# Performance work log

Hardware: AMD Instinct MI355X
Metric: run time of the kernel (lower is better)

The kernel has to match this reference:

```python
import jax, jax.numpy as jnp
import numpy as np

EPS_BN = 1e-5
EPS_LN = 1e-5


def _conv1d(x, w, b, pad):
    # x: (B, Cin, L), w: (Cout, Cin, K)
    y = jax.lax.conv_general_dilated(x, w, window_strides=(1,), padding=[(pad, pad)],
                                     dimension_numbers=('NCH', 'OIH', 'NCH'))
    return y + b[None, :, None]


def _bn_eval(x, g, b, m, v):
    return (x - m[None, :, None]) * (g / jnp.sqrt(v + EPS_BN))[None, :, None] + b[None, :, None]


def _maxpool2(x):
    B, C, L = x.shape
    return x.reshape(B, C, L // 2, 2).max(-1)


def _wavelet(x, t, s, w):
    # x: (B, In); t, s, w: (Out, In); mexican_hat wavelet
    z = (x[:, None, :] - t[None]) / (s + 1e-8)  # (B, Out, In)
    wav = (1.0 - z * z) * jnp.exp(-0.5 * z * z)
    return jnp.einsum('boi,oi->bo', wav, w)


def _ln(x, g, b):
    m = x.mean(-1, keepdims=True)
    v = ((x - m) ** 2).mean(-1, keepdims=True)
    return (x - m) / jnp.sqrt(v + EPS_LN) * g + b


def setup_inputs() -> dict:
    key = jax.random.key(0)
    ks = iter(jax.random.split(key, 40))
    B, L = 1024, 1024
    R = 64                 # repr_dim
    KIN = 128 * (R // 4)   # 2048 = conv stem flattened features
    d = {}
    d['x'] = jax.random.normal(next(ks), (B, 1, L), jnp.float32)
    for i, (ci, co, k) in enumerate([(1, 32, 7), (32, 64, 5), (64, 128, 3)], 1):
        fan = ci * k
        d[f'conv{i}_w'] = jax.random.normal(next(ks), (co, ci, k), jnp.float32) / np.sqrt(fan)
        d[f'conv{i}_b'] = jnp.zeros((co,), jnp.float32)
        d[f'bn{i}_g'] = jnp.ones((co,), jnp.float32)
        d[f'bn{i}_b'] = jnp.zeros((co,), jnp.float32)
        d[f'bn{i}_m'] = jax.random.normal(next(ks), (co,), jnp.float32) * 0.1
        d[f'bn{i}_v'] = jax.random.uniform(next(ks), (co,), jnp.float32, 0.5, 1.5)
    for i, fin in enumerate([KIN, R, R], 1):
        d[f'wl{i}_t'] = jax.random.uniform(next(ks), (R, fin), jnp.float32, -1.0, 1.0)
        d[f'wl{i}_s'] = jax.random.uniform(next(ks), (R, fin), jnp.float32, 0.1, 1.0)
        d[f'wl{i}_w'] = jax.random.normal(next(ks), (R, fin), jnp.float32) / np.sqrt(fin)
        d[f'ln{i}_g'] = jnp.ones((R,), jnp.float32)
        d[f'ln{i}_b'] = jnp.zeros((R,), jnp.float32)
    return d


def _forward(x, p):
    h = _conv1d(x, p['conv1_w'], p['conv1_b'], 3)
    h = jax.nn.gelu(_bn_eval(h, p['bn1_g'], p['bn1_b'], p['bn1_m'], p['bn1_v']), approximate=False)
    h = _maxpool2(h)
    h = _conv1d(h, p['conv2_w'], p['conv2_b'], 2)
    h = jax.nn.gelu(_bn_eval(h, p['bn2_g'], p['bn2_b'], p['bn2_m'], p['bn2_v']), approximate=False)
    h = _maxpool2(h)
    h = _conv1d(h, p['conv3_w'], p['conv3_b'], 1)
    h = jax.nn.gelu(_bn_eval(h, p['bn3_g'], p['bn3_b'], p['bn3_m'], p['bn3_v']), approximate=False)
    # AdaptiveAvgPool1d(16): L=256 splits evenly into 16 bins of 16
    B, C, L = h.shape
    h = h.reshape(B, C, 16, L // 16).mean(-1)
    feat = h.reshape(B, -1)  # (B, 2048)
    for i in (1, 2, 3):
        feat = _ln(jax.nn.silu(_wavelet(feat, p[f'wl{i}_t'], p[f'wl{i}_s'], p[f'wl{i}_w'])),
                   p[f'ln{i}_g'], p[f'ln{i}_b'])
    return feat  # (B, 64)


def reference(x, conv1_w, conv1_b, bn1_g, bn1_b, bn1_m, bn1_v,
              conv2_w, conv2_b, bn2_g, bn2_b, bn2_m, bn2_v,
              conv3_w, conv3_b, bn3_g, bn3_b, bn3_m, bn3_v,
              wl1_t, wl1_s, wl1_w, ln1_g, ln1_b,
              wl2_t, wl2_s, wl2_w, ln2_g, ln2_b,
              wl3_t, wl3_s, wl3_w, ln3_g, ln3_b):
    p = dict(locals())
    p.pop('x')
    return _forward(x, p)
```

## Files before the change

### kernel.cpp

```cpp
#include <hip/hip_runtime.h>
#include <hip/hip_bf16.h>
#include <math.h>

#define WS_W2H   0
#define WS_W2L   5120
#define WS_W3H   10240
#define WS_W3L   23040
#define WS_A1    35840
#define WS_C1    35872
#define WS_A2    35904
#define WS_C2    35968
#define WS_A3    36032
#define WS_C3    36160
#define WS_T1T   36288
#define WS_IS1T  167360
#define WS_WW1T  298432
#define WS_T2T   429504
#define WS_IS2T  433600
#define WS_WW2T  437696
#define WS_T3T   441792
#define WS_IS3T  445888
#define WS_WW3T  449984
#define WS_H2H   454080
#define WS_H2L   8842688
#define WS_FEAT  17231296

typedef _Float16 f16x8 __attribute__((ext_vector_type(8)));
typedef float    f32x4 __attribute__((ext_vector_type(4)));

struct InPtrs { const float* p[34]; };

__device__ __forceinline__ float gelu_fast(float x) {
    float z  = 0.70710678118654752f * x;
    float az = fabsf(z);
    float t  = __builtin_amdgcn_rcpf(fmaf(0.3275911f, az, 1.0f));
    float p  = fmaf(1.061405429f, t, -1.453152027f);
    p = fmaf(p, t, 1.421413741f);
    p = fmaf(p, t, -0.284496736f);
    p = fmaf(p, t, 0.254829592f);
    p = p * t;
    float e  = __expf(-z * z);
    float erf_abs = fmaf(-p, e, 1.0f);
    float erfv = copysignf(erf_abs, z);
    return 0.5f * x * (1.0f + erfv);
}

__global__ __launch_bounds__(256) void prep_kernel(InPtrs in, float* __restrict__ ws) {
    int idx = blockIdx.x * 256 + threadIdx.x;
    if (idx >= 453856) return;
    if (idx < 10240) {
        int co = idx / 160; int kk = idx - co * 160;
        int tap = kk >> 5, ci = kk & 31;
        float val = in.p[7][co * 160 + ci * 5 + tap];
        _Float16 hi = (_Float16)val;
        ((_Float16*)(ws + WS_W2H))[co * 160 + kk] = hi;
        ((_Float16*)(ws + WS_W2L))[co * 160 + kk] = (_Float16)(val - (float)hi);
    } else if (idx < 35840) {
        int n = idx - 10240;
        int co = n / 200; int k = n - co * 200;
        float val = 0.0f;
        if (k < 192) { int ci = k & 63; int tap = k >> 6; val = in.p[13][co * 192 + ci * 3 + tap]; }
        _Float16 hi = (_Float16)val;
        ((_Float16*)(ws + WS_W3H))[co * 200 + k] = hi;
        ((_Float16*)(ws + WS_W3L))[co * 200 + k] = (_Float16)(val - (float)hi);
    } else if (idx < 36064) {
        int n = idx - 35840;
        int ch, offA, offC; const float *cb, *g, *bb, *m, *v;
        if (n < 32)      { ch = n;      cb = in.p[2];  g = in.p[3];  bb = in.p[4];  m = in.p[5];  v = in.p[6];  offA = WS_A1; offC = WS_C1; }
        else if (n < 96) { ch = n - 32; cb = in.p[8];  g = in.p[9];  bb = in.p[10]; m = in.p[11]; v = in.p[12]; offA = WS_A2; offC = WS_C2; }
        else             { ch = n - 96; cb = in.p[14]; g = in.p[15]; bb = in.p[16]; m = in.p[17]; v = in.p[18]; offA = WS_A3; offC = WS_C3; }
        float A = g[ch] * rsqrtf(v[ch] + 1e-5f);
        ws[offA + ch] = A;
        ws[offC + ch] = (cb[ch] - m[ch]) * A + bb[ch];
    } else if (idx < 429280) {
        int n = idx - 36064;
        int arr = n / 131072; int m = n - arr * 131072;
        int o = m >> 11; int i = m & 2047;
        float val = in.p[19 + arr][o * 2048 + i];
        if (arr == 1) val = 1.0f / (val + 1e-8f);
        int base = (arr == 0) ? WS_T1T : (arr == 1) ? WS_IS1T : WS_WW1T;
        ws[base + i * 64 + o] = val;
    } else {
        int n = idx - 429280;
        int layer = n / 12288; int m = n - layer * 12288;
        int arr = m / 4096; int mm = m - arr * 4096;
        int o = mm >> 6; int i = mm & 63;
        float val = in.p[(layer == 0 ? 24 : 29) + arr][o * 64 + i];
        if (arr == 1) val = 1.0f / (val + 1e-8f);
        int base;
        if (layer == 0) base = (arr == 0) ? WS_T2T : (arr == 1) ? WS_IS2T : WS_WW2T;
        else            base = (arr == 0) ? WS_T3T : (arr == 1) ? WS_IS3T : WS_WW3T;
        ws[base + i * 64 + o] = val;
    }
}

__global__ __launch_bounds__(256) void k12m_kernel(const float* __restrict__ x,
                                                   const float* __restrict__ w1,
                                                   const float* __restrict__ ws,
                                                   _Float16* __restrict__ h2h,
                                                   _Float16* __restrict__ h2l) {
    __shared__ float xs[528];
    __shared__ float w1s[224];
    __shared__ float a1s[32], c1s[32], a2s[64], c2s[64];
    __shared__ __align__(16) _Float16 h1h[260 * 40];
    __shared__ __align__(16) _Float16 h1l[260 * 40];

    int t = threadIdx.x;
    int b = blockIdx.x >> 1, q = blockIdx.x & 1;
    int xoff = 512 * q - 7;

    for (int j = t; j < 526; j += 256) {
        int gx = xoff + j;
        xs[j] = (gx >= 0 && gx < 1024) ? x[b * 1024 + gx] : 0.0f;
    }
    if (t < 224) w1s[t] = w1[t];
    if (t < 32) { a1s[t] = ws[WS_A1 + t]; c1s[t] = ws[WS_C1 + t]; }
    if (t < 64) { a2s[t] = ws[WS_A2 + t]; c2s[t] = ws[WS_C2 + t]; }
    __syncthreads();

    for (int item = t; item < 260 * 32; item += 256) {
        int r = item >> 5, ci = item & 31;
        int hp = 256 * q - 2 + r;
        float val = 0.0f;
        if (hp >= 0 && hp < 512) {
            float d0 = 0.0f, d1 = 0.0f;
            #pragma unroll
            for (int k = 0; k < 7; ++k) {
                float w = w1s[ci * 7 + k];
                d0 += w * xs[2 * r + k];
                d1 += w * xs[2 * r + k + 1];
            }
            float A = a1s[ci], C = c1s[ci];
            val = fmaxf(gelu_fast(d0 * A + C), gelu_fast(d1 * A + C));
        }
        _Float16 hi = (_Float16)val;
        h1h[r * 40 + ci] = hi;
        h1l[r * 40 + ci] = (_Float16)(val - (float)hi);
    }
    __syncthreads();

    int w = t >> 6, lane = t & 63;
    int m = lane & 15, quad = lane >> 4;
    const _Float16* w2h = (const _Float16*)(ws + WS_W2H);
    const _Float16* w2l = (const _Float16*)(ws + WS_W2L);

    f32x4 acc[4][4] = {};
    #pragma unroll
    for (int s = 0; s < 5; ++s) {
        f16x8 ah[4], al[4], bh[4], bl[4];
        #pragma unroll
        for (int tr = 0; tr < 4; ++tr) {
            int rloc = 64 * w + 16 * tr + m + s;
            ah[tr] = *(const f16x8*)(&h1h[rloc * 40 + quad * 8]);
            al[tr] = *(const f16x8*)(&h1l[rloc * 40 + quad * 8]);
        }
        #pragma unroll
        for (int tc = 0; tc < 4; ++tc) {
            int off = (16 * tc + m) * 160 + 32 * s + quad * 8;
            bh[tc] = *(const f16x8*)(w2h + off);
            bl[tc] = *(const f16x8*)(w2l + off);
        }
        #pragma unroll
        for (int tr = 0; tr < 4; ++tr)
            #pragma unroll
            for (int tc = 0; tc < 4; ++tc) {
                acc[tr][tc] = __builtin_amdgcn_mfma_f32_16x16x32_f16(ah[tr], bh[tc], acc[tr][tc], 0, 0, 0);
                acc[tr][tc] = __builtin_amdgcn_mfma_f32_16x16x32_f16(al[tr], bh[tc], acc[tr][tc], 0, 0, 0);
                acc[tr][tc] = __builtin_amdgcn_mfma_f32_16x16x32_f16(ah[tr], bl[tc], acc[tr][tc], 0, 0, 0);
            }
    }

    #pragma unroll
    for (int tc = 0; tc < 4; ++tc) {
        int co = 16 * tc + m;
        float A2 = a2s[co], C2 = c2s[co];
        #pragma unroll
        for (int tr = 0; tr < 4; ++tr) {
            float g0 = gelu_fast(acc[tr][tc][0] * A2 + C2);
            float g1 = gelu_fast(acc[tr][tc][1] * A2 + C2);
            float g2 = gelu_fast(acc[tr][tc][2] * A2 + C2);
            float g3 = gelu_fast(acc[tr][tc][3] * A2 + C2);
            float p0 = fmaxf(g0, g1), p1 = fmaxf(g2, g3);
            int rowl0 = 64 * w + 16 * tr + quad * 4;
            int lp = 128 * q + (rowl0 >> 1);
            size_t i0 = ((size_t)b * 256 + lp) * 64 + co;
            _Float16 h0 = (_Float16)p0, h1v = (_Float16)p1;
            h2h[i0] = h0;       h2l[i0] = (_Float16)(p0 - (float)h0);
            h2h[i0 + 64] = h1v; h2l[i0 + 64] = (_Float16)(p1 - (float)h1v);
        }
    }
}

__global__ __launch_bounds__(256) void k3m_kernel(const _Float16* __restrict__ h2h,
                                                  const _Float16* __restrict__ h2l,
                                                  const _Float16* __restrict__ w3h,
                                                  const _Float16* __restrict__ w3l,
                                                  const float* __restrict__ ws,
                                                  float* __restrict__ feat) {
    __shared__ __align__(16) _Float16 Ah[130 * 88];
    __shared__ __align__(16) _Float16 Al[130 * 88];

    int t = threadIdx.x;
    int b = blockIdx.x >> 1, q = blockIdx.x & 1;
    int l0 = q * 128;

    for (int item = t; item < 130 * 8; item += 256) {
        int r = item >> 3, seg = item & 7;
        int l = l0 - 1 + r;
        uint4 vh = make_uint4(0u, 0u, 0u, 0u), vl = vh;
        if (l >= 0 && l < 256) {
            size_t base = ((size_t)b * 256 + l) * 64;
            vh = *((const uint4*)(h2h + base) + seg);
            vl = *((const uint4*)(h2l + base) + seg);
        }
        *(uint4*)(&Ah[r * 88 + seg * 8]) = vh;
        *(uint4*)(&Al[r * 88 + seg * 8]) = vl;
    }
    __syncthreads();

    int w = t >> 6, lane = t & 63;
    int wr = w >> 1, wc = w & 1;
    int m = lane & 15, quad = lane >> 4;

    f32x4 acc[4][4] = {};
    size_t boff = (size_t)(wc * 64 + m) * 200 + quad * 8;

    #pragma unroll
    for (int s = 0; s < 6; ++s) {
        int kbase = s * 32;
        int k = kbase + quad * 8;
        int koff = k >> 6, ci = k & 63;
        f16x8 ah[4], al[4], bh[4], bl[4];
        #pragma unroll
        for (int tr = 0; tr < 4; ++tr) {
            int row = 64 * wr + 16 * tr + m;
            ah[tr] = *(const f16x8*)(&Ah[(row + koff) * 88 + ci]);
            al[tr] = *(const f16x8*)(&Al[(row + koff) * 88 + ci]);
        }
        #pragma unroll
        for (int tc = 0; tc < 4; ++tc) {
            bh[tc] = *(const f16x8*)(w3h + boff + 16 * tc * 200 + kbase);
            bl[tc] = *(const f16x8*)(w3l + boff + 16 * tc * 200 + kbase);
        }
        #pragma unroll
        for (int tr = 0; tr < 4; ++tr)
            #pragma unroll
            for (int tc = 0; tc < 4; ++tc) {
                acc[tr][tc] = __builtin_amdgcn_mfma_f32_16x16x32_f16(ah[tr], bh[tc], acc[tr][tc], 0, 0, 0);
                acc[tr][tc] = __builtin_amdgcn_mfma_f32_16x16x32_f16(al[tr], bh[tc], acc[tr][tc], 0, 0, 0);
                acc[tr][tc] = __builtin_amdgcn_mfma_f32_16x16x32_f16(ah[tr], bl[tc], acc[tr][tc], 0, 0, 0);
            }
    }

    #pragma unroll
    for (int tc = 0; tc < 4; ++tc) {
        int co = 64 * wc + 16 * tc + m;
        float A3 = ws[WS_A3 + co], C3 = ws[WS_C3 + co];
        #pragma unroll
        for (int tr = 0; tr < 4; ++tr) {
            float s = 0.0f;
            #pragma unroll
            for (int r = 0; r < 4; ++r)
                s += gelu_fast(acc[tr][tc][r] * A3 + C3);
            s += __shfl_xor(s, 16, 64);
            s += __shfl_xor(s, 32, 64);
            if (quad == 0) {
                int bin = (l0 >> 4) + 4 * wr + tr;
                feat[(size_t)b * 2048 + co * 16 + bin] = s * 0.0625f;
            }
        }
    }
}

__device__ __forceinline__ float wave_sum(float v) {
    #pragma unroll
    for (int off = 32; off > 0; off >>= 1) v += __shfl_xor(v, off, 64);
    return v;
}
__device__ __forceinline__ float silu_f(float v) {
    return v / (1.0f + __expf(-v));
}

__global__ __launch_bounds__(1024) void k4_kernel(const float* __restrict__ ws,
        const float* __restrict__ ln1g, const float* __restrict__ ln1b,
        const float* __restrict__ ln2g, const float* __restrict__ ln2b,
        const float* __restrict__ ln3g, const float* __restrict__ ln3b,
        float* __restrict__ out) {
    __shared__ __align__(16) float fs[4 * 2048];
    __shared__ float red[16 * 256];

    int t = threadIdx.x;
    int b0 = blockIdx.x * 4;
    const float* feat = ws + WS_FEAT;
    {
        const float4* src = (const float4*)(feat + (size_t)b0 * 2048);
        float4* dst = (float4*)fs;
        for (int i = t; i < 2048; i += 1024) dst[i] = src[i];
    }
    __syncthreads();

    int o = t & 63, grp = t >> 6;
    const float* t1t  = ws + WS_T1T;
    const float* is1t = ws + WS_IS1T;
    const float* w1t  = ws + WS_WW1T;
    float acc0 = 0.0f, acc1 = 0.0f, acc2 = 0.0f, acc3 = 0.0f;
    int i0 = grp * 128;
    for (int i = i0; i < i0 + 128; ++i) {
        float tv = t1t[i * 64 + o], sv = is1t[i * 64 + o], wv = w1t[i * 64 + o];
        float z, z2;
        z = (fs[i] - tv) * sv;        z2 = z * z; acc0 += (1.0f - z2) * __expf(-0.5f * z2) * wv;
        z = (fs[2048 + i] - tv) * sv; z2 = z * z; acc1 += (1.0f - z2) * __expf(-0.5f * z2) * wv;
        z = (fs[4096 + i] - tv) * sv; z2 = z * z; acc2 += (1.0f - z2) * __expf(-0.5f * z2) * wv;
        z = (fs[6144 + i] - tv) * sv; z2 = z * z; acc3 += (1.0f - z2) * __expf(-0.5f * z2) * wv;
    }
    red[grp * 256 + 0 * 64 + o] = acc0;
    red[grp * 256 + 1 * 64 + o] = acc1;
    red[grp * 256 + 2 * 64 + o] = acc2;
    red[grp * 256 + 3 * 64 + o] = acc3;
    __syncthreads();

    if (grp < 4) {
        int w = grp;
        float y = 0.0f;
        #pragma unroll
        for (int j = 0; j < 16; ++j) y += red[j * 256 + w * 64 + o];

        y = silu_f(y);
        float m = wave_sum(y) * 0.015625f;
        float d = y - m;
        float var = wave_sum(d * d) * 0.015625f;
        float yn = d * rsqrtf(var + 1e-5f) * ln1g[o] + ln1b[o];

        {
            const float* t2t  = ws + WS_T2T;
            const float* is2t = ws + WS_IS2T;
            const float* w2t  = ws + WS_WW2T;
            float a = 0.0f;
            for (int i = 0; i < 64; ++i) {
                float xi = __shfl(yn, i, 64);
                float tv = t2t[i * 64 + o], sv = is2t[i * 64 + o], wv = w2t[i * 64 + o];
                float z = (xi - tv) * sv, z2 = z * z;
                a += (1.0f - z2) * __expf(-0.5f * z2) * wv;
            }
            float y2 = silu_f(a);
            float m2 = wave_sum(y2) * 0.015625f;
            float d2 = y2 - m2;
            float v2 = wave_sum(d2 * d2) * 0.015625f;
            yn = d2 * rsqrtf(v2 + 1e-5f) * ln2g[o] + ln2b[o];
        }
        {
            const float* t3t  = ws + WS_T3T;
            const float* is3t = ws + WS_IS3T;
            const float* w3t  = ws + WS_WW3T;
            float a = 0.0f;
            for (int i = 0; i < 64; ++i) {
                float xi = __shfl(yn, i, 64);
                float tv = t3t[i * 64 + o], sv = is3t[i * 64 + o], wv = w3t[i * 64 + o];
                float z = (xi - tv) * sv, z2 = z * z;
                a += (1.0f - z2) * __expf(-0.5f * z2) * wv;
            }
            float y3 = silu_f(a);
            float m3 = wave_sum(y3) * 0.015625f;
            float d3 = y3 - m3;
            float v3 = wave_sum(d3 * d3) * 0.015625f;
            yn = d3 * rsqrtf(v3 + 1e-5f) * ln3g[o] + ln3b[o];
        }
        out[((size_t)b0 + w) * 64 + o] = yn;
    }
}

extern "C" void kernel_launch(void* const* d_in, const int* in_sizes, int n_in,
                              void* d_out, int out_size, void* d_ws, size_t ws_size,
                              hipStream_t stream) {
    float* ws = (float*)d_ws;
    InPtrs ip;
    for (int i = 0; i < 34; ++i) ip.p[i] = (const float*)d_in[i];

    prep_kernel<<<1774, 256, 0, stream>>>(ip, ws);
    k12m_kernel<<<2048, 256, 0, stream>>>((const float*)d_in[0], (const float*)d_in[1],
                                          ws,
                                          (_Float16*)(ws + WS_H2H),
                                          (_Float16*)(ws + WS_H2L));
    k3m_kernel<<<2048, 256, 0, stream>>>((const _Float16*)(ws + WS_H2H),
                                         (const _Float16*)(ws + WS_H2L),
                                         (const _Float16*)(ws + WS_W3H),
                                         (const _Float16*)(ws + WS_W3L),
                                         ws, ws + WS_FEAT);
    k4_kernel<<<256, 1024, 0, stream>>>(ws,
        (const float*)d_in[22], (const float*)d_in[23],
        (const float*)d_in[27], (const float*)d_in[28],
        (const float*)d_in[32], (const float*)d_in[33],
        (float*)d_out);
}
```

Baseline: 299.5 us.

## Fuse conv1/conv2 kernel with conv3 kernel via halo recompute in LDS

Merges the conv1+conv2 kernel and the conv3 kernel into one kernel that keeps the conv2 output (hi/lo fp16 split) in shared memory instead of writing it to global workspace. Each block recomputes a slightly larger halo of conv1/conv2 rows, using an extra 16-row MFMA tile on wave 0, so conv3 has its boundary rows locally. This removes the global round trip of the large intermediate and one kernel launch. In exchange it adds redundant halo compute, an unbalanced extra tile on one wave, and more accumulator registers, which may lower occupancy.

```diff
diff --git a/kernel.cpp b/kernel.cpp
--- a/kernel.cpp
+++ b/kernel.cpp
@@ -21,9 +21,7 @@
 #define WS_T3T   441792
 #define WS_IS3T  445888
 #define WS_WW3T  449984
-#define WS_H2H   454080
-#define WS_H2L   8842688
-#define WS_FEAT  17231296
+#define WS_FEAT  454080
 
 typedef _Float16 f16x8 __attribute__((ext_vector_type(8)));
 typedef float    f32x4 __attribute__((ext_vector_type(4)));
@@ -94,23 +92,25 @@
     }
 }
 
-__global__ __launch_bounds__(256) void k12m_kernel(const float* __restrict__ x,
-                                                   const float* __restrict__ w1,
-                                                   const float* __restrict__ ws,
-                                                   _Float16* __restrict__ h2h,
-                                                   _Float16* __restrict__ h2l) {
-    __shared__ float xs[528];
+__global__ __launch_bounds__(256) void kconv_kernel(const float* __restrict__ x,
+                                                    const float* __restrict__ w1,
+                                                    const float* __restrict__ ws,
+                                                    const _Float16* __restrict__ w3h,
+                                                    const _Float16* __restrict__ w3l,
+                                                    float* __restrict__ feat) {
+    __shared__ float xs[560];
     __shared__ float w1s[224];
     __shared__ float a1s[32], c1s[32], a2s[64], c2s[64];
-    __shared__ __align__(16) _Float16 h1h[260 * 40];
-    __shared__ __align__(16) _Float16 h1l[260 * 40];
+    __shared__ __align__(16) _Float16 U[2 * 276 * 40];
+
+    _Float16* h1h = U;
+    _Float16* h1l = U + 276 * 40;
 
     int t = threadIdx.x;
     int b = blockIdx.x >> 1, q = blockIdx.x & 1;
-    int xoff = 512 * q - 7;
-
-    for (int j = t; j < 526; j += 256) {
-        int gx = xoff + j;
+
+    for (int j = t; j < 558; j += 256) {
+        int gx = 512 * q - 11 + j;
         xs[j] = (gx >= 0 && gx < 1024) ? x[b * 1024 + gx] : 0.0f;
     }
     if (t < 224) w1s[t] = w1[t];
@@ -118,9 +118,9 @@
     if (t < 64) { a2s[t] = ws[WS_A2 + t]; c2s[t] = ws[WS_C2 + t]; }
     __syncthreads();
 
-    for (int item = t; item < 260 * 32; item += 256) {
+    for (int item = t; item < 276 * 32; item += 256) {
         int r = item >> 5, ci = item & 31;
-        int hp = 256 * q - 2 + r;
+        int hp = 256 * q - 4 + r;
         float val = 0.0f;
         if (hp >= 0 && hp < 512) {
             float d0 = 0.0f, d1 = 0.0f;
@@ -141,19 +141,14 @@
 
     int w = t >> 6, lane = t & 63;
     int m = lane & 15, quad = lane >> 4;
+
     const _Float16* w2h = (const _Float16*)(ws + WS_W2H);
     const _Float16* w2l = (const _Float16*)(ws + WS_W2L);
-
-    f32x4 acc[4][4] = {};
+    f32x4 acc[5][4] = {};
+
     #pragma unroll
     for (int s = 0; s < 5; ++s) {
-        f16x8 ah[4], al[4], bh[4], bl[4];
-        #pragma unroll
-        for (int tr = 0; tr < 4; ++tr) {
-            int rloc = 64 * w + 16 * tr + m + s;
-            ah[tr] = *(const f16x8*)(&h1h[rloc * 40 + quad * 8]);
-            al[tr] = *(const f16x8*)(&h1l[rloc * 40 + quad * 8]);
-        }
+        f16x8 bh[4], bl[4];
         #pragma unroll
         for (int tc = 0; tc < 4; ++tc) {
             int off = (16 * tc + m) * 160 + 32 * s + quad * 8;
@@ -161,68 +156,58 @@
             bl[tc] = *(const f16x8*)(w2l + off);
         }
         #pragma unroll
-        for (int tr = 0; tr < 4; ++tr)
+        for (int i = 0; i < 5; ++i) {
+            if (i == 4 && w != 0) continue;
+            int fr = (i < 4) ? (4 * i + w) : 16;
+            f16x8 ah = *(const f16x8*)(&h1h[(16 * fr + m + s) * 40 + quad * 8]);
+            f16x8 al = *(const f16x8*)(&h1l[(16 * fr + m + s) * 40 + quad * 8]);
             #pragma unroll
             for (int tc = 0; tc < 4; ++tc) {
-                acc[tr][tc] = __builtin_amdgcn_mfma_f32_16x16x32_f16(ah[tr], bh[tc], acc[tr][tc], 0, 0, 0);
-                acc[tr][tc] = __builtin_amdgcn_mfma_f32_16x16x32_f16(al[tr], bh[tc], acc[tr][tc], 0, 0, 0);
-                acc[tr][tc] = __builtin_amdgcn_mfma_f32_16x16x32_f16(ah[tr], bl[tc], acc[tr][tc], 0, 0, 0);
-            }
-    }
-
-    #pragma unroll
-    for (int tc = 0; tc < 4; ++tc) {
-        int co = 16 * tc + m;
-        float A2 = a2s[co], C2 = c2s[co];
-        #pragma unroll
-        for (int tr = 0; tr < 4; ++tr) {
-            float g0 = gelu_fast(acc[tr][tc][0] * A2 + C2);
-            float g1 = gelu_fast(acc[tr][tc][1] * A2 + C2);
-            float g2 = gelu_fast(acc[tr][tc][2] * A2 + C2);
-            float g3 = gelu_fast(acc[tr][tc][3] * A2 + C2);
+                acc[i][tc] = __builtin_amdgcn_mfma_f32_16x16x32_f16(ah, bh[tc], acc[i][tc], 0, 0, 0);
+                acc[i][tc] = __builtin_amdgcn_mfma_f32_16x16x32_f16(al, bh[tc], acc[i][tc], 0, 0, 0);
+                acc[i][tc] = __builtin_amdgcn_mfma_f32_16x16x32_f16(ah, bl[tc], acc[i][tc], 0, 0, 0);
+            }
+        }
+    }
+    __syncthreads();
+
+    _Float16* h2h = U;
+    _Float16* h2l = U + 130 * 72;
+    if (q == 0 && t < 64) { h2h[0 * 72 + t]   = (_Float16)0.f; h2l[0 * 72 + t]   = (_Float16)0.f; }
+    if (q == 1 && t < 64) { h2h[129 * 72 + t] = (_Float16)0.f; h2l[129 * 72 + t] = (_Float16)0.f; }
+
+    #pragma unroll
+    for (int i = 0; i < 5; ++i) {
+        if (i == 4 && w != 0) continue;
+        int fr = (i < 4) ? (4 * i + w) : 16;
+        #pragma unroll
+        for (int tc = 0; tc < 4; ++tc) {
+            int co = 16 * tc + m;
+            float A2 = a2s[co], C2 = c2s[co];
+            float g0 = gelu_fast(acc[i][tc][0] * A2 + C2);
+            float g1 = gelu_fast(acc[i][tc][1] * A2 + C2);
+            float g2 = gelu_fast(acc[i][tc][2] * A2 + C2);
+            float g3 = gelu_fast(acc[i][tc][3] * A2 + C2);
             float p0 = fmaxf(g0, g1), p1 = fmaxf(g2, g3);
-            int rowl0 = 64 * w + 16 * tr + quad * 4;
-            int lp = 128 * q + (rowl0 >> 1);
-            size_t i0 = ((size_t)b * 256 + lp) * 64 + co;
-            _Float16 h0 = (_Float16)p0, h1v = (_Float16)p1;
-            h2h[i0] = h0;       h2l[i0] = (_Float16)(p0 - (float)h0);
-            h2h[i0 + 64] = h1v; h2l[i0 + 64] = (_Float16)(p1 - (float)h1v);
-        }
-    }
-}
-
-__global__ __launch_bounds__(256) void k3m_kernel(const _Float16* __restrict__ h2h,
-                                                  const _Float16* __restrict__ h2l,
-                                                  const _Float16* __restrict__ w3h,
-                                                  const _Float16* __restrict__ w3l,
-                                                  const float* __restrict__ ws,
-                                                  float* __restrict__ feat) {
-    __shared__ __align__(16) _Float16 Ah[130 * 88];
-    __shared__ __align__(16) _Float16 Al[130 * 88];
-
-    int t = threadIdx.x;
-    int b = blockIdx.x >> 1, q = blockIdx.x & 1;
-    int l0 = q * 128;
-
-    for (int item = t; item < 130 * 8; item += 256) {
-        int r = item >> 3, seg = item & 7;
-        int l = l0 - 1 + r;
-        uint4 vh = make_uint4(0u, 0u, 0u, 0u), vl = vh;
-        if (l >= 0 && l < 256) {
-            size_t base = ((size_t)b * 256 + l) * 64;
-            vh = *((const uint4*)(h2h + base) + seg);
-            vl = *((const uint4*)(h2l + base) + seg);
-        }
-        *(uint4*)(&Ah[r * 88 + seg * 8]) = vh;
-        *(uint4*)(&Al[r * 88 + seg * 8]) = vl;
-    }
-    __syncthreads();
-
-    int w = t >> 6, lane = t & 63;
+            int ll0 = 8 * fr + 2 * quad;
+            int lg0 = 128 * q - 1 + ll0;
+            if (ll0 < 130 && (unsigned)lg0 < 256u) {
+                _Float16 h0 = (_Float16)p0;
+                h2h[ll0 * 72 + co] = h0;
+                h2l[ll0 * 72 + co] = (_Float16)(p0 - (float)h0);
+            }
+            int ll1 = ll0 + 1, lg1 = lg0 + 1;
+            if (ll1 < 130 && (unsigned)lg1 < 256u) {
+                _Float16 h1v = (_Float16)p1;
+                h2h[ll1 * 72 + co] = h1v;
+                h2l[ll1 * 72 + co] = (_Float16)(p1 - (float)h1v);
+            }
+        }
+    }
+    __syncthreads();
+
     int wr = w >> 1, wc = w & 1;
-    int m = lane & 15, quad = lane >> 4;
-
-    f32x4 acc[4][4] = {};
+    f32x4 acc2[4][4] = {};
     size_t boff = (size_t)(wc * 64 + m) * 200 + quad * 8;
 
     #pragma unroll
@@ -234,8 +219,8 @@
         #pragma unroll
         for (int tr = 0; tr < 4; ++tr) {
             int row = 64 * wr + 16 * tr + m;
-            ah[tr] = *(const f16x8*)(&Ah[(row + koff) * 88 + ci]);
-            al[tr] = *(const f16x8*)(&Al[(row + koff) * 88 + ci]);
+            ah[tr] = *(const f16x8*)(&h2h[(row + koff) * 72 + ci]);
+            al[tr] = *(const f16x8*)(&h2l[(row + koff) * 72 + ci]);
         }
         #pragma unroll
         for (int tc = 0; tc < 4; ++tc) {
@@ -246,9 +231,9 @@
         for (int tr = 0; tr < 4; ++tr)
             #pragma unroll
             for (int tc = 0; tc < 4; ++tc) {
-                acc[tr][tc] = __builtin_amdgcn_mfma_f32_16x16x32_f16(ah[tr], bh[tc], acc[tr][tc], 0, 0, 0);
-                acc[tr][tc] = __builtin_amdgcn_mfma_f32_16x16x32_f16(al[tr], bh[tc], acc[tr][tc], 0, 0, 0);
-                acc[tr][tc] = __builtin_amdgcn_mfma_f32_16x16x32_f16(ah[tr], bl[tc], acc[tr][tc], 0, 0, 0);
+                acc2[tr][tc] = __builtin_amdgcn_mfma_f32_16x16x32_f16(ah[tr], bh[tc], acc2[tr][tc], 0, 0, 0);
+                acc2[tr][tc] = __builtin_amdgcn_mfma_f32_16x16x32_f16(al[tr], bh[tc], acc2[tr][tc], 0, 0, 0);
+                acc2[tr][tc] = __builtin_amdgcn_mfma_f32_16x16x32_f16(ah[tr], bl[tc], acc2[tr][tc], 0, 0, 0);
             }
     }
 
@@ -261,11 +246,11 @@
             float s = 0.0f;
             #pragma unroll
             for (int r = 0; r < 4; ++r)
-                s += gelu_fast(acc[tr][tc][r] * A3 + C3);
+                s += gelu_fast(acc2[tr][tc][r] * A3 + C3);
             s += __shfl_xor(s, 16, 64);
             s += __shfl_xor(s, 32, 64);
             if (quad == 0) {
-                int bin = (l0 >> 4) + 4 * wr + tr;
+                int bin = 8 * q + 4 * wr + tr;
                 feat[(size_t)b * 2048 + co * 16 + bin] = s * 0.0625f;
             }
         }
@@ -377,15 +362,11 @@
     for (int i = 0; i < 34; ++i) ip.p[i] = (const float*)d_in[i];
 
     prep_kernel<<<1774, 256, 0, stream>>>(ip, ws);
-    k12m_kernel<<<2048, 256, 0, stream>>>((const float*)d_in[0], (const float*)d_in[1],
-                                          ws,
-                                          (_Float16*)(ws + WS_H2H),
-                                          (_Float16*)(ws + WS_H2L));
-    k3m_kernel<<<2048, 256, 0, stream>>>((const _Float16*)(ws + WS_H2H),
-                                         (const _Float16*)(ws + WS_H2L),
-                                         (const _Float16*)(ws + WS_W3H),
-                                         (const _Float16*)(ws + WS_W3L),
-                                         ws, ws + WS_FEAT);
+    kconv_kernel<<<2048, 256, 0, stream>>>((const float*)d_in[0], (const float*)d_in[1],
+                                           ws,
+                                           (const _Float16*)(ws + WS_W3H),
+                                           (const _Float16*)(ws + WS_W3L),
+                                           ws + WS_FEAT);
     k4_kernel<<<256, 1024, 0, stream>>>(ws,
         (const float*)d_in[22], (const float*)d_in[23],
         (const float*)d_in[27], (const float*)d_in[28],
```

Result: slower. 318.9 us (+6.5%).
